# Optimization experiments

Measured on AMD Instinct MI355X. Metric: run time of the kernel, lower is better.

Reference implementation:

```python
import jax, jax.numpy as jnp
import numpy as np

INF = 100000000.0
TOPK = 13
ALPHA = 1
BETA = 6


def box_cxcywh_to_xyxy(b):
    cx, cy, w, h = jnp.split(b, 4, axis=-1)
    return jnp.concatenate([cx - 0.5 * w, cy - 0.5 * h, cx + 0.5 * w, cy + 0.5 * h], axis=-1)


def generalized_box_iou(boxes1, boxes2):
    # boxes1: [N,4] xyxy, boxes2: [G,4] xyxy -> [N,G]
    area1 = (boxes1[:, 2] - boxes1[:, 0]) * (boxes1[:, 3] - boxes1[:, 1])
    area2 = (boxes2[:, 2] - boxes2[:, 0]) * (boxes2[:, 3] - boxes2[:, 1])
    lt = jnp.maximum(boxes1[:, None, :2], boxes2[None, :, :2])
    rb = jnp.minimum(boxes1[:, None, 2:], boxes2[None, :, 2:])
    wh = jnp.clip(rb - lt, 0.0)
    inter = wh[..., 0] * wh[..., 1]
    union = area1[:, None] + area2[None, :] - inter
    iou = inter / union
    lt_e = jnp.minimum(boxes1[:, None, :2], boxes2[None, :, :2])
    rb_e = jnp.maximum(boxes1[:, None, 2:], boxes2[None, :, 2:])
    wh_e = jnp.clip(rb_e - lt_e, 0.0)
    area_e = wh_e[..., 0] * wh_e[..., 1]
    return iou - (area_e - union) / area_e


def _assign_one(cls_logits, bbox_pred, gt_boxes, gt_labels):
    # cls_logits [N,C], bbox_pred [N,4] cxcywh, gt_boxes [G,4] cxcywh, gt_labels [G]
    N = bbox_pred.shape[0]
    G = gt_boxes.shape[0]
    scores = jax.nn.sigmoid(cls_logits)
    overlaps = -generalized_box_iou(box_cxcywh_to_xyxy(bbox_pred), box_cxcywh_to_xyxy(gt_boxes))  # [N,G]
    bbox_scores = scores[:, gt_labels]                       # [N,G] gather per-gt class score
    alignment = bbox_scores ** ALPHA * overlaps ** BETA      # [N,G]
    # per-gt topk over queries
    cand_metrics, cand_idxs = jax.lax.top_k(alignment.T, TOPK)  # [G,K]
    is_pos = cand_metrics > 0
    vals = jnp.take_along_axis(overlaps.T, cand_idxs, axis=1)   # [G,K]
    rows = jnp.broadcast_to(jnp.arange(G)[:, None], (G, TOPK))
    cols = jnp.where(is_pos, cand_idxs, N)  # out-of-bounds col -> dropped
    oinf = jnp.full((G, N), -INF, dtype=overlaps.dtype)
    oinf = oinf.at[rows, cols].set(vals, mode='drop')
    max_overlaps = oinf.max(axis=0)     # [N]
    argmax_overlaps = oinf.argmax(axis=0)
    pos = max_overlaps != -INF
    assigned_gt_inds = jnp.where(pos, argmax_overlaps + 1, 0)
    assign_metrics = jnp.where(pos, alignment[jnp.arange(N), argmax_overlaps], 0.0)
    assigned_labels = jnp.where(pos, gt_labels[argmax_overlaps], -1)
    return assigned_gt_inds, assigned_labels, assign_metrics


def setup_inputs() -> dict:
    key = jax.random.key(0)
    k1, k2, k3, k4 = jax.random.split(key, 4)
    bs, N, C, G = 16, 4000, 80, 300
    return {
        'pred_logits': jax.random.normal(k1, (bs, N, C), dtype=jnp.float32),
        'pred_boxes': jax.random.uniform(k2, (bs, N, 4), dtype=jnp.float32, minval=0.05, maxval=0.95),
        'gt_boxes': jax.random.uniform(k3, (bs, G, 4), dtype=jnp.float32, minval=0.05, maxval=0.95),
        'gt_labels': jax.random.randint(k4, (bs, G), 0, C),
    }


def reference(pred_logits, pred_boxes, gt_boxes, gt_labels):
    # Fixed-shape equivalent of matched_list: assigned_gt_inds[b,q] == 0 means
    # background; k>0 means query q matched to gt k-1 (same semantics as the
    # (valid_query_idx, valid_assigned_gt_inds) pairs in the torch code).
    return jax.vmap(_assign_one)(pred_logits, pred_boxes, gt_boxes, gt_labels)
```

## Files before the change

### kernel.cpp

```cpp
#include <hip/hip_runtime.h>

#define NPRED  4000
#define NGROUP 1000
#define NGT    300
#define NCLS   80
#define TOPKK  13
#define NCHUNK 125

typedef unsigned long long u64;

__device__ __forceinline__ float frcp(float x) { return __builtin_amdgcn_rcpf(x); }
__device__ __forceinline__ float fexp(float x) {
    return __builtin_amdgcn_exp2f(x * 1.44269504088896341f);
}

__device__ __forceinline__ float neg_giou_pa(float4 p, float pa, float gx1, float gy1,
                                             float gx2, float gy2, float garea) {
    float whx = fmaxf(fminf(p.z, gx2) - fmaxf(p.x, gx1), 0.0f);
    float why = fmaxf(fminf(p.w, gy2) - fmaxf(p.y, gy1), 0.0f);
    float inter = whx * why;
    float uni = pa + garea - inter;
    float iou = inter * frcp(uni);
    float wex = fmaxf(p.z, gx2) - fminf(p.x, gx1);
    float wey = fmaxf(p.w, gy2) - fminf(p.y, gy1);
    float area_e = wex * wey;
    return (area_e - uni) * frcp(area_e) - iou;
}

__device__ __forceinline__ float4 to_xyxy(float4 pb) {
    return make_float4(pb.x - 0.5f * pb.z, pb.y - 0.5f * pb.w,
                       pb.x + 0.5f * pb.z, pb.y + 0.5f * pb.w);
}

__device__ __forceinline__ float sigmoid_fast(float x) {
    return frcp(1.0f + fexp(-x));
}

__device__ __forceinline__ float pow6(float x) {
    float x2 = x * x;
    float x4 = x2 * x2;
    return x2 * x4;
}

__device__ __forceinline__ unsigned ord_float(float f) {
    unsigned u = __float_as_uint(f);
    return u ^ ((unsigned)(((int)u) >> 31) | 0x80000000u);
}

__device__ __forceinline__ u64 pack_key(float v, int n) {
    return ((u64)__float_as_uint(v) << 32) | (u64)(~(unsigned)n);
}

__global__ void init_keys(u64* keys, int n) {
    int i = blockIdx.x * blockDim.x + threadIdx.x;
    if (i < n) keys[i] = 0ULL;
}

__global__ __launch_bounds__(256) void sig_transpose(const float* __restrict__ logits,
                                                     const float4* __restrict__ pboxes,
                                                     float* __restrict__ st,
                                                     float4* __restrict__ pxyxy,
                                                     float* __restrict__ parea,
                                                     u64* __restrict__ keys,
                                                     int total_keys) {
    const int tid = threadIdx.x;
    const int gid = blockIdx.x * 256 + tid;
    if (gid < total_keys) keys[gid] = 0ULL;

    const int b = blockIdx.x / NCHUNK;
    const int n0 = (blockIdx.x % NCHUNK) * 32;

    if (tid < 32) {
        int n = n0 + tid;
        float4 x = to_xyxy(pboxes[(size_t)b * NPRED + n]);
        pxyxy[(size_t)b * NPRED + n] = x;
        parea[(size_t)b * NPRED + n] = (x.z - x.x) * (x.w - x.y);
    }

    __shared__ float tile[NCLS][32 + 1];

    const float4* src = (const float4*)(logits + ((size_t)b * NPRED + n0) * NCLS);
    #pragma unroll
    for (int it = 0; it < 3; ++it) {
        int i4 = tid + it * 256;
        if (i4 < 640) {
            int p = i4 / 20;
            int c = (i4 - p * 20) * 4;
            float4 v = src[i4];
            tile[c + 0][p] = sigmoid_fast(v.x);
            tile[c + 1][p] = sigmoid_fast(v.y);
            tile[c + 2][p] = sigmoid_fast(v.z);
            tile[c + 3][p] = sigmoid_fast(v.w);
        }
    }
    __syncthreads();
    float* dstbase = st + (size_t)b * NCLS * NPRED + n0;
    #pragma unroll
    for (int it = 0; it < 3; ++it) {
        int w4 = tid + it * 256;
        if (w4 < 640) {
            int c = w4 >> 3, r4 = (w4 & 7) * 4;
            float4 v = make_float4(tile[c][r4], tile[c][r4 + 1],
                                   tile[c][r4 + 2], tile[c][r4 + 3]);
            *(float4*)(dstbase + (size_t)c * NPRED + r4) = v;
        }
    }
}

template <bool PRE>
__global__ __launch_bounds__(256) void topk_scatter(const float* __restrict__ logits,
                                                    const float* __restrict__ st,
                                                    const float4* __restrict__ pboxes,
                                                    const float4* __restrict__ pxyxy,
                                                    const float* __restrict__ parea,
                                                    const float4* __restrict__ gboxes,
                                                    const int* __restrict__ glabels,
                                                    u64* __restrict__ keys) {
    const int blk = blockIdx.x;
    const int b = blk / NGT;
    const int g = blk - b * NGT;
    const int tid = threadIdx.x;
    const int wave = tid >> 6;
    const int lane = tid & 63;

    __shared__ __align__(16) float s_key[NPRED];
    __shared__ u64 s_wave[4];
    __shared__ u64 s_win[TOPKK];

    float4 gb = gboxes[b * NGT + g];
    const int lab = glabels[b * NGT + g];
    const float gx1 = gb.x - 0.5f * gb.z;
    const float gy1 = gb.y - 0.5f * gb.w;
    const float gx2 = gb.x + 0.5f * gb.z;
    const float gy2 = gb.y + 0.5f * gb.w;
    const float garea = (gx2 - gx1) * (gy2 - gy1);

    const float* lg = logits + (size_t)b * NPRED * NCLS + lab;
    const float* srow = st + ((size_t)b * NCLS + lab) * NPRED;
    const float4* srow4 = (const float4*)srow;
    const float4* par4 = (const float4*)(parea + (size_t)b * NPRED);
    const float4* pbb = pboxes + (size_t)b * NPRED;
    const float4* pxr = pxyxy + (size_t)b * NPRED;

    u64 b1 = 0ULL, b2 = 0ULL;
    #pragma unroll
    for (int j = 0; j < 4; ++j) {
        int grp = tid + j * 256;
        if (grp < NGROUP) {
            int n0 = grp * 4;
            float s0, s1, s2, s3;
            float4 p0, p1, p2, p3;
            float a0, a1, a2, a3;
            if (PRE) {
                float4 s4 = srow4[grp];
                s0 = s4.x; s1 = s4.y; s2 = s4.z; s3 = s4.w;
                float4 a4 = par4[grp];
                a0 = a4.x; a1 = a4.y; a2 = a4.z; a3 = a4.w;
                p0 = pxr[n0]; p1 = pxr[n0 + 1]; p2 = pxr[n0 + 2]; p3 = pxr[n0 + 3];
            } else {
                s0 = sigmoid_fast(lg[(size_t)(n0 + 0) * NCLS]);
                s1 = sigmoid_fast(lg[(size_t)(n0 + 1) * NCLS]);
                s2 = sigmoid_fast(lg[(size_t)(n0 + 2) * NCLS]);
                s3 = sigmoid_fast(lg[(size_t)(n0 + 3) * NCLS]);
                p0 = to_xyxy(pbb[n0]);     p1 = to_xyxy(pbb[n0 + 1]);
                p2 = to_xyxy(pbb[n0 + 2]); p3 = to_xyxy(pbb[n0 + 3]);
                a0 = (p0.z - p0.x) * (p0.w - p0.y);
                a1 = (p1.z - p1.x) * (p1.w - p1.y);
                a2 = (p2.z - p2.x) * (p2.w - p2.y);
                a3 = (p3.z - p3.x) * (p3.w - p3.y);
            }
            float v0 = s0 * pow6(neg_giou_pa(p0, a0, gx1, gy1, gx2, gy2, garea));
            float v1 = s1 * pow6(neg_giou_pa(p1, a1, gx1, gy1, gx2, gy2, garea));
            float v2 = s2 * pow6(neg_giou_pa(p2, a2, gx1, gy1, gx2, gy2, garea));
            float v3 = s3 * pow6(neg_giou_pa(p3, a3, gx1, gy1, gx2, gy2, garea));
            *(float4*)&s_key[n0] = make_float4(v0, v1, v2, v3);
            u64 k0 = pack_key(v0, n0);
            u64 k1 = pack_key(v1, n0 + 1);
            u64 k2 = pack_key(v2, n0 + 2);
            u64 k3 = pack_key(v3, n0 + 3);
            if (k0 > b1) { b2 = b1; b1 = k0; } else if (k0 > b2) b2 = k0;
            if (k1 > b1) { b2 = b1; b1 = k1; } else if (k1 > b2) b2 = k1;
            if (k2 > b1) { b2 = b1; b1 = k2; } else if (k2 > b2) b2 = k2;
            if (k3 > b1) { b2 = b1; b1 = k3; } else if (k3 > b2) b2 = k3;
        }
    }

    {
        u64 m1 = b1;
        #pragma unroll
        for (int m = 1; m < 64; m <<= 1) {
            u64 o = __shfl_xor(m1, m, 64);
            if (o > m1) m1 = o;
        }
        if (lane == 0) s_wave[wave] = m1;
    }

    int nwin = 0;
    for (int k = 0; k < TOPKK; ++k) {
        __syncthreads();
        u64 t1 = s_wave[0];
        u64 c;
        c = s_wave[1]; if (c > t1) t1 = c;
        c = s_wave[2]; if (c > t1) t1 = c;
        c = s_wave[3]; if (c > t1) t1 = c;
        if ((unsigned)(t1 >> 32) == 0u) break;
        if (tid == 0) s_win[k] = t1;
        nwin = k + 1;
        int n1 = (int)(~(unsigned)t1);
        int ownerTid = (n1 >> 2) & 255;
        if (tid == ownerTid) {
            s_key[n1] = 0.0f;
            if (b2 != 0ULL) { b1 = b2; b2 = 0ULL; }
            else {
                b1 = 0ULL;
                #pragma unroll
                for (int jj = 0; jj < 4; ++jj) {
                    int grp = tid + jj * 256;
                    if (grp >= NGROUP) continue;
                    int n0 = grp * 4;
                    float4 q = *(const float4*)&s_key[n0];
                    u64 c0 = pack_key(q.x, n0);
                    u64 c1 = pack_key(q.y, n0 + 1);
                    u64 c2 = pack_key(q.z, n0 + 2);
                    u64 c3 = pack_key(q.w, n0 + 3);
                    if (c0 > b1) { b2 = b1; b1 = c0; } else if (c0 > b2) b2 = c0;
                    if (c1 > b1) { b2 = b1; b1 = c1; } else if (c1 > b2) b2 = c1;
                    if (c2 > b1) { b2 = b1; b1 = c2; } else if (c2 > b2) b2 = c2;
                    if (c3 > b1) { b2 = b1; b1 = c3; } else if (c3 > b2) b2 = c3;
                }
            }
        }
        if ((ownerTid >> 6) == wave) {
            u64 m1 = b1;
            #pragma unroll
            for (int m = 1; m < 64; m <<= 1) {
                u64 o = __shfl_xor(m1, m, 64);
                if (o > m1) m1 = o;
            }
            if (lane == 0) s_wave[wave] = m1;
        }
    }
    __syncthreads();

    if (tid < nwin) {
        u64 t = s_win[tid];
        int wi = (int)(~(unsigned)t);
        float4 p;
        if (PRE) p = pxr[wi];
        else     p = to_xyxy(pbb[wi]);
        float pa = (p.z - p.x) * (p.w - p.y);
        float o = neg_giou_pa(p, pa, gx1, gy1, gx2, gy2, garea);
        unsigned mbits = (unsigned)(t >> 32) >> 16;
        u64 key = ((u64)ord_float(o) << 32)
                | ((u64)(511u - (unsigned)g) << 23)
                | ((u64)mbits << 7);
        atomicMax(&keys[(size_t)b * NPRED + wi], key);
    }
}

__global__ void finalize(const int* __restrict__ glabels,
                         const u64* __restrict__ keys,
                         float* __restrict__ out, int total) {
    int i = blockIdx.x * blockDim.x + threadIdx.x;
    if (i >= total) return;
    int b = i / NPRED;
    u64 key = keys[i];
    float o0 = 0.0f, o1 = -1.0f, o2 = 0.0f;
    if (key != 0ULL) {
        int g = 511 - (int)((key >> 23) & 0x1FF);
        o0 = (float)(g + 1);
        o1 = (float)glabels[b * NGT + g];
        o2 = __uint_as_float(((unsigned)(key >> 7) & 0xFFFFu) << 16);
    }
    out[i] = o0;
    out[(size_t)total + i] = o1;
    out[(size_t)2 * total + i] = o2;
}

extern "C" void kernel_launch(void* const* d_in, const int* in_sizes, int n_in,
                              void* d_out, int out_size, void* d_ws, size_t ws_size,
                              hipStream_t stream) {
    const float* logits  = (const float*)d_in[0];
    const float4* pboxes = (const float4*)d_in[1];
    const float4* gboxes = (const float4*)d_in[2];
    const int* glabels   = (const int*)d_in[3];

    const int bs = in_sizes[3] / NGT;
    const int total = bs * NPRED;
    char* ws = (char*)d_ws;
    u64* keys   = (u64*)ws;                    ws += (size_t)total * 8;
    float* st   = (float*)ws;                  ws += (size_t)bs * NCLS * NPRED * 4;
    float4* pxy = (float4*)ws;                 ws += (size_t)total * 16;
    float* par  = (float*)ws;                  ws += (size_t)total * 4;
    float* out = (float*)d_out;

    const size_t need = (size_t)(ws - (char*)d_ws);
    if (ws_size >= need) {
        sig_transpose<<<bs * NCHUNK, 256, 0, stream>>>(logits, pboxes, st, pxy,
                                                       par, keys, total);
        topk_scatter<true><<<bs * NGT, 256, 0, stream>>>(logits, st, pboxes, pxy,
                                                         par, gboxes, glabels, keys);
    } else {
        init_keys<<<(total + 255) / 256, 256, 0, stream>>>(keys, total);
        topk_scatter<false><<<bs * NGT, 256, 0, stream>>>(logits, st, pboxes, pxy,
                                                          par, gboxes, glabels, keys);
    }
    finalize<<<(total + 255) / 256, 256, 0, stream>>>(glabels, keys, out, total);
}
```

Measured before the change: 123.1 us.

## Cache per-wave maxima in registers and cut barriers in top-k selection loop

Each thread now keeps the four per-wave maxima in registers. Each round the owning wave publishes its new maximum to a per-round shared slot, so one barrier per round replaces the repeated shared reads. The last round skips the refill work, and winners are held in a per-thread register rather than a shared array. The initial best-two tracking uses separate float and index registers instead of 64-bit keys, which lowers the integer compare cost in the main scan. The risk is a change in tie handling, since the packed-key compare broke ties by index while the float compare keeps the first seen.

Measured after the change: 129.2 us. 5.0% more time.

```diff
diff --git a/kernel.cpp b/kernel.cpp
--- a/kernel.cpp
+++ b/kernel.cpp
@@ -50,6 +50,8 @@
 __device__ __forceinline__ u64 pack_key(float v, int n) {
     return ((u64)__float_as_uint(v) << 32) | (u64)(~(unsigned)n);
 }
+
+__device__ __forceinline__ u64 umax64(u64 a, u64 b) { return a > b ? a : b; }
 
 __global__ void init_keys(u64* keys, int n) {
     int i = blockIdx.x * blockDim.x + threadIdx.x;
@@ -125,7 +127,7 @@
 
     __shared__ __align__(16) float s_key[NPRED];
     __shared__ u64 s_wave[4];
-    __shared__ u64 s_win[TOPKK];
+    __shared__ u64 s_rnd[TOPKK];
 
     float4 gb = gboxes[b * NGT + g];
     const int lab = glabels[b * NGT + g];
@@ -142,7 +144,8 @@
     const float4* pbb = pboxes + (size_t)b * NPRED;
     const float4* pxr = pxyxy + (size_t)b * NPRED;
 
-    u64 b1 = 0ULL, b2 = 0ULL;
+    float bv1 = -1.0f, bv2 = -1.0f;
+    int   bn1 = 0,     bn2 = 0;
     #pragma unroll
     for (int j = 0; j < 4; ++j) {
         int grp = tid + j * 256;
@@ -174,16 +177,18 @@
             float v2 = s2 * pow6(neg_giou_pa(p2, a2, gx1, gy1, gx2, gy2, garea));
             float v3 = s3 * pow6(neg_giou_pa(p3, a3, gx1, gy1, gx2, gy2, garea));
             *(float4*)&s_key[n0] = make_float4(v0, v1, v2, v3);
-            u64 k0 = pack_key(v0, n0);
-            u64 k1 = pack_key(v1, n0 + 1);
-            u64 k2 = pack_key(v2, n0 + 2);
-            u64 k3 = pack_key(v3, n0 + 3);
-            if (k0 > b1) { b2 = b1; b1 = k0; } else if (k0 > b2) b2 = k0;
-            if (k1 > b1) { b2 = b1; b1 = k1; } else if (k1 > b2) b2 = k1;
-            if (k2 > b1) { b2 = b1; b1 = k2; } else if (k2 > b2) b2 = k2;
-            if (k3 > b1) { b2 = b1; b1 = k3; } else if (k3 > b2) b2 = k3;
-        }
-    }
+            if (v0 > bv1) { bv2 = bv1; bn2 = bn1; bv1 = v0; bn1 = n0; }
+            else if (v0 > bv2) { bv2 = v0; bn2 = n0; }
+            if (v1 > bv1) { bv2 = bv1; bn2 = bn1; bv1 = v1; bn1 = n0 + 1; }
+            else if (v1 > bv2) { bv2 = v1; bn2 = n0 + 1; }
+            if (v2 > bv1) { bv2 = bv1; bn2 = bn1; bv1 = v2; bn1 = n0 + 2; }
+            else if (v2 > bv2) { bv2 = v2; bn2 = n0 + 2; }
+            if (v3 > bv1) { bv2 = bv1; bn2 = bn1; bv1 = v3; bn1 = n0 + 3; }
+            else if (v3 > bv2) { bv2 = v3; bn2 = n0 + 3; }
+        }
+    }
+    u64 b1 = pack_key(bv1, bn1);
+    u64 b2 = pack_key(bv2, bn2);
 
     {
         u64 m1 = b1;
@@ -194,56 +199,65 @@
         }
         if (lane == 0) s_wave[wave] = m1;
     }
-
+    __syncthreads();
+    u64 w0c = s_wave[0], w1c = s_wave[1], w2c = s_wave[2], w3c = s_wave[3];
+
+    u64 mywin = 0ULL;
     int nwin = 0;
     for (int k = 0; k < TOPKK; ++k) {
-        __syncthreads();
-        u64 t1 = s_wave[0];
-        u64 c;
-        c = s_wave[1]; if (c > t1) t1 = c;
-        c = s_wave[2]; if (c > t1) t1 = c;
-        c = s_wave[3]; if (c > t1) t1 = c;
+        u64 t1 = umax64(umax64(w0c, w1c), umax64(w2c, w3c));
         if ((unsigned)(t1 >> 32) == 0u) break;
-        if (tid == 0) s_win[k] = t1;
+        if (tid == k) mywin = t1;
         nwin = k + 1;
+        if (k == TOPKK - 1) break;
         int n1 = (int)(~(unsigned)t1);
         int ownerTid = (n1 >> 2) & 255;
-        if (tid == ownerTid) {
-            s_key[n1] = 0.0f;
-            if (b2 != 0ULL) { b1 = b2; b2 = 0ULL; }
-            else {
-                b1 = 0ULL;
-                #pragma unroll
-                for (int jj = 0; jj < 4; ++jj) {
-                    int grp = tid + jj * 256;
-                    if (grp >= NGROUP) continue;
-                    int n0 = grp * 4;
-                    float4 q = *(const float4*)&s_key[n0];
-                    u64 c0 = pack_key(q.x, n0);
-                    u64 c1 = pack_key(q.y, n0 + 1);
-                    u64 c2 = pack_key(q.z, n0 + 2);
-                    u64 c3 = pack_key(q.w, n0 + 3);
-                    if (c0 > b1) { b2 = b1; b1 = c0; } else if (c0 > b2) b2 = c0;
-                    if (c1 > b1) { b2 = b1; b1 = c1; } else if (c1 > b2) b2 = c1;
-                    if (c2 > b1) { b2 = b1; b1 = c2; } else if (c2 > b2) b2 = c2;
-                    if (c3 > b1) { b2 = b1; b1 = c3; } else if (c3 > b2) b2 = c3;
+        int ow = (n1 >> 8) & 3;
+        u64 wv = 0ULL;
+        if (wave == ow) {
+            if (tid == ownerTid) {
+                s_key[n1] = 0.0f;
+                if (b2 != 0ULL) { b1 = b2; b2 = 0ULL; }
+                else {
+                    b1 = 0ULL;
+                    #pragma unroll
+                    for (int jj = 0; jj < 4; ++jj) {
+                        int grp = tid + jj * 256;
+                        if (grp >= NGROUP) continue;
+                        int n0 = grp * 4;
+                        float4 q = *(const float4*)&s_key[n0];
+                        u64 c0 = pack_key(q.x, n0);
+                        u64 c1 = pack_key(q.y, n0 + 1);
+                        u64 c2 = pack_key(q.z, n0 + 2);
+                        u64 c3 = pack_key(q.w, n0 + 3);
+                        if (c0 > b1) { b2 = b1; b1 = c0; } else if (c0 > b2) b2 = c0;
+                        if (c1 > b1) { b2 = b1; b1 = c1; } else if (c1 > b2) b2 = c1;
+                        if (c2 > b1) { b2 = b1; b1 = c2; } else if (c2 > b2) b2 = c2;
+                        if (c3 > b1) { b2 = b1; b1 = c3; } else if (c3 > b2) b2 = c3;
+                    }
                 }
             }
-        }
-        if ((ownerTid >> 6) == wave) {
-            u64 m1 = b1;
+            wv = b1;
             #pragma unroll
             for (int m = 1; m < 64; m <<= 1) {
-                u64 o = __shfl_xor(m1, m, 64);
-                if (o > m1) m1 = o;
+                u64 o = __shfl_xor(wv, m, 64);
+                if (o > wv) wv = o;
             }
-            if (lane == 0) s_wave[wave] = m1;
-        }
-    }
-    __syncthreads();
+            if (lane == 0) s_rnd[k] = wv;
+        }
+        __syncthreads();
+        u64 upd;
+        if (wave == ow) upd = wv;
+        else            upd = s_rnd[k];
+        int ows = __builtin_amdgcn_readfirstlane(ow);
+        if (ows == 0)      w0c = upd;
+        else if (ows == 1) w1c = upd;
+        else if (ows == 2) w2c = upd;
+        else               w3c = upd;
+    }
 
     if (tid < nwin) {
-        u64 t = s_win[tid];
+        u64 t = mywin;
         int wi = (int)(~(unsigned)t);
         float4 p;
         if (PRE) p = pxr[wi];
```

## Do per-wave top-k selection independently, then merge four sorted candidate lists

Applied to the files above, without the earlier changes.

Each wave now extracts its own top-13 candidates using only wave shuffles, with no block-wide barrier per iteration. The four sorted per-wave lists are written to shared memory once and merged with a small 4-way merge that every thread runs redundantly. This removes 13 __syncthreads rounds and the cross-wave serial dependency. In exchange each wave does up to 13 shuffle reductions of its own instead of only the owning wave refreshing, and the final merge adds serial shared-memory reads.

Result: slower. 136.5 us (+10.9%).

```diff
diff --git a/kernel.cpp b/kernel.cpp
--- a/kernel.cpp
+++ b/kernel.cpp
@@ -50,6 +50,8 @@
 __device__ __forceinline__ u64 pack_key(float v, int n) {
     return ((u64)__float_as_uint(v) << 32) | (u64)(~(unsigned)n);
 }
+
+__device__ __forceinline__ u64 umax64(u64 a, u64 b) { return a > b ? a : b; }
 
 __global__ void init_keys(u64* keys, int n) {
     int i = blockIdx.x * blockDim.x + threadIdx.x;
@@ -124,8 +126,7 @@
     const int lane = tid & 63;
 
     __shared__ __align__(16) float s_key[NPRED];
-    __shared__ u64 s_wave[4];
-    __shared__ u64 s_win[TOPKK];
+    __shared__ __align__(16) u64 s_cand[4 * TOPKK];
 
     float4 gb = gboxes[b * NGT + g];
     const int lab = glabels[b * NGT + g];
@@ -185,30 +186,23 @@
         }
     }
 
-    {
-        u64 m1 = b1;
+    u64 mywin = 0ULL;
+    int nw = 0;
+    #pragma unroll 1
+    for (int k = 0; k < TOPKK; ++k) {
+        u64 w = b1;
         #pragma unroll
         for (int m = 1; m < 64; m <<= 1) {
-            u64 o = __shfl_xor(m1, m, 64);
-            if (o > m1) m1 = o;
-        }
-        if (lane == 0) s_wave[wave] = m1;
-    }
-
-    int nwin = 0;
-    for (int k = 0; k < TOPKK; ++k) {
-        __syncthreads();
-        u64 t1 = s_wave[0];
-        u64 c;
-        c = s_wave[1]; if (c > t1) t1 = c;
-        c = s_wave[2]; if (c > t1) t1 = c;
-        c = s_wave[3]; if (c > t1) t1 = c;
-        if ((unsigned)(t1 >> 32) == 0u) break;
-        if (tid == 0) s_win[k] = t1;
-        nwin = k + 1;
-        int n1 = (int)(~(unsigned)t1);
-        int ownerTid = (n1 >> 2) & 255;
-        if (tid == ownerTid) {
+            u64 o = __shfl_xor(w, m, 64);
+            if (o > w) w = o;
+        }
+        if ((unsigned)(w >> 32) == 0u) break;
+        if (lane == k) mywin = w;
+        nw = k + 1;
+        if (k == TOPKK - 1) break;
+        int n1 = (int)(~(unsigned)w);
+        int ownerLane = (n1 >> 2) & 63;
+        if (lane == ownerLane) {
             s_key[n1] = 0.0f;
             if (b2 != 0ULL) { b1 = b2; b2 = 0ULL; }
             else {
@@ -230,20 +224,31 @@
                 }
             }
         }
-        if ((ownerTid >> 6) == wave) {
-            u64 m1 = b1;
-            #pragma unroll
-            for (int m = 1; m < 64; m <<= 1) {
-                u64 o = __shfl_xor(m1, m, 64);
-                if (o > m1) m1 = o;
-            }
-            if (lane == 0) s_wave[wave] = m1;
-        }
-    }
+    }
+    if (lane < TOPKK)
+        s_cand[wave * TOPKK + lane] = (lane < nw) ? mywin : 0ULL;
     __syncthreads();
 
+    u64 c0 = s_cand[0], c1 = s_cand[TOPKK],
+        c2 = s_cand[2 * TOPKK], c3 = s_cand[3 * TOPKK];
+    int h1 = 0, h2 = 0, h3 = 0, h0 = 0;
+    u64 mw = 0ULL;
+    int nwin = 0;
+    #pragma unroll 1
+    for (int i = 0; i < TOPKK; ++i) {
+        u64 h = umax64(umax64(c0, c1), umax64(c2, c3));
+        if ((unsigned)(h >> 32) == 0u) break;
+        if (tid == i) mw = h;
+        nwin = i + 1;
+        if (i == TOPKK - 1) break;
+        if (h == c0)      { ++h0; c0 = (h0 < TOPKK) ? s_cand[h0] : 0ULL; }
+        else if (h == c1) { ++h1; c1 = (h1 < TOPKK) ? s_cand[TOPKK + h1] : 0ULL; }
+        else if (h == c2) { ++h2; c2 = (h2 < TOPKK) ? s_cand[2 * TOPKK + h2] : 0ULL; }
+        else              { ++h3; c3 = (h3 < TOPKK) ? s_cand[3 * TOPKK + h3] : 0ULL; }
+    }
+
     if (tid < nwin) {
-        u64 t = s_win[tid];
+        u64 t = mw;
         int wi = (int)(~(unsigned)t);
         float4 p;
         if (PRE) p = pxr[wi];
```
